# Kernel tuning notes

Hardware: AMD Instinct MI355X
Metric: run time of the kernel (lower is better)

Reference implementation:

```python
import jax, jax.numpy as jnp
import numpy as np

B, N, D, H = 1, 4096, 1024, 16
E = D // H  # head_dim = 64


def setup_inputs() -> dict:
    key = jax.random.key(0)
    ks = jax.random.split(key, 5)
    s = 0.02
    return {
        "query": jax.random.normal(ks[0], (B, N, D), dtype=jnp.float32),
        "Wq": jax.random.normal(ks[1], (D, D), dtype=jnp.float32) * s,
        "Wk": jax.random.normal(ks[2], (D, D), dtype=jnp.float32) * s,
        "Wv": jax.random.normal(ks[3], (D, D), dtype=jnp.float32) * s,
        "Wo": jax.random.normal(ks[4], (D, D), dtype=jnp.float32) * s,
        "bo": jnp.zeros((D,), dtype=jnp.float32),
    }


def reference(query, Wq, Wk, Wv, Wo, bo):
    # self-attention: key = value = query
    # nn.Linear: y = x @ W.T  (weights stored as [out, in])
    q = query @ Wq.T  # [b, n, d]
    k = query @ Wk.T
    v = query @ Wv.T
    # 'b n (h e) -> b h n e'
    q = q.reshape(B, N, H, E).transpose(0, 2, 1, 3)
    k = k.reshape(B, N, H, E).transpose(0, 2, 1, 3)
    v = v.reshape(B, N, H, E).transpose(0, 2, 1, 3)
    scale = 1.0 / jnp.sqrt(jnp.asarray(E, dtype=q.dtype))
    attn = jnp.einsum('bhne,bhme->bhnm', q, k) * scale  # [b, h, n, n]
    attn = jax.nn.softmax(attn, axis=-1)
    out = jnp.einsum('bhnm,bhme->bhne', attn, v)  # [b, h, n, e]
    # 'b h n e -> b n (h e)'
    out = out.transpose(0, 2, 1, 3).reshape(B, N, D)
    out = out @ Wo.T + bo
    return out
```

## Files before the change

### kernel.cpp

```cpp
#include <hip/hip_runtime.h>


typedef __attribute__((ext_vector_type(8))) __bf16 bf16x8;
typedef __attribute__((ext_vector_type(4))) float f32x4;
typedef __attribute__((ext_vector_type(16))) float f32x16;
typedef __attribute__((ext_vector_type(4))) unsigned short us4;
typedef __attribute__((ext_vector_type(4))) unsigned int u32x4;
typedef __attribute__((ext_vector_type(2))) unsigned int u32x2;

#define DEV __device__ __forceinline__

#define QSCALE 0.1803368801111204f

DEV unsigned short f2bf(float x) {
  union { float f; unsigned u; } c; c.f = x;
  unsigned u = c.u;
  u += 0x7FFFu + ((u >> 16) & 1u);
  return (unsigned short)(u >> 16);
}

DEV float expq(float x) {
#if __has_builtin(__builtin_amdgcn_exp2f)
  return __builtin_amdgcn_exp2f(x);
#else
  float r;
  asm("v_exp_f32 %0, %1" : "=v"(r) : "v"(x));
  return r;
#endif
}

DEV unsigned cvtpk_bf16(float lo, float hi) {
  unsigned r;
  asm("v_cvt_pk_bf16_f32 %0, %1, %2" : "=v"(r) : "v"(lo), "v"(hi));
  return r;
}

DEV void plswap_u(unsigned& a, unsigned& b) {
#if __has_builtin(__builtin_amdgcn_permlane32_swap)
  u32x2 r = __builtin_amdgcn_permlane32_swap(a, b, false, false);
  a = r.x; b = r.y;
#else
  asm("v_permlane32_swap_b32 %0, %1" : "+v"(a), "+v"(b));
#endif
}

DEV void gload16(const void* g, void* lds) {
  __builtin_amdgcn_global_load_lds(
      (const __attribute__((address_space(1))) unsigned int*)g,
      (__attribute__((address_space(3))) unsigned int*)lds, 16, 0, 0);
}

__global__ void cast_all(const float* __restrict__ q,
                         const float* __restrict__ wa,
                         const float* __restrict__ wb,
                         const float* __restrict__ wc,
                         const float* __restrict__ wd,
                         unsigned short* __restrict__ qo,
                         unsigned short* __restrict__ wout) {
  const int y = blockIdx.y;
  const int i = blockIdx.x * 256 + threadIdx.x;
  const float* src;
  unsigned short* dst;
  if (y < 4) {
    src = q + (size_t)y * 1048576;
    dst = qo + (size_t)y * 1048576;
  } else {
    src = (y == 4) ? wa : (y == 5) ? wb : (y == 6) ? wc : wd;
    dst = wout + (size_t)(y - 4) * 1048576;
  }
  float4 v = reinterpret_cast<const float4*>(src)[i];
  us4 o;
  o.x = f2bf(v.x); o.y = f2bf(v.y); o.z = f2bf(v.z); o.w = f2bf(v.w);
  reinterpret_cast<us4*>(dst)[i] = o;
}

__global__ __launch_bounds__(256)
void gemm_qkv(const unsigned short* __restrict__ A,
              const unsigned short* __restrict__ B,
              unsigned short* __restrict__ Qo,
              unsigned short* __restrict__ Ko,
              unsigned short* __restrict__ Vo) {
  constexpr int K = 1024, BK = 64;
  __shared__ unsigned short As[128 * BK];
  __shared__ unsigned short Bs[128 * BK];
  const int t = threadIdx.x;
  const int w = t >> 6, l = t & 63;
  const int brow = blockIdx.x * 128;
  const int bcol = blockIdx.y * 128;
  const int wr = w >> 1, wc = w & 1;
  const int lr = l >> 3;
  const int lc = ((l & 7) ^ lr) * 8;
  const int fr = l & 15;
  const int fcb = (l >> 4) * 16;
  const int swz = (l & 7) << 4;

  f32x4 acc[4][4] = {};
  const char* Asb = (const char*)As;
  const char* Bsb = (const char*)Bs;

  for (int k0 = 0; k0 < K; k0 += BK) {
#pragma unroll
    for (int i = 0; i < 4; ++i) {
      const int r = w * 32 + i * 8;
      gload16(A + (size_t)(brow + r + lr) * K + k0 + lc, (void*)(As + r * BK));
      gload16(B + (size_t)(bcol + r + lr) * K + k0 + lc, (void*)(Bs + r * BK));
    }
    __syncthreads();
#pragma unroll
    for (int kk = 0; kk < 2; ++kk) {
      bf16x8 af[4], bfr[4];
#pragma unroll
      for (int m = 0; m < 4; ++m)
        af[m] = *(const bf16x8*)(Asb + (wr * 64 + m * 16 + fr) * 128 +
                                 ((kk * 64 + fcb) ^ swz));
#pragma unroll
      for (int n = 0; n < 4; ++n)
        bfr[n] = *(const bf16x8*)(Bsb + (wc * 64 + n * 16 + fr) * 128 +
                                  ((kk * 64 + fcb) ^ swz));
#pragma unroll
      for (int m = 0; m < 4; ++m)
#pragma unroll
        for (int n = 0; n < 4; ++n)
          acc[m][n] = __builtin_amdgcn_mfma_f32_16x16x32_bf16(
              af[m], bfr[n], acc[m][n], 0, 0, 0);
    }
    __syncthreads();
  }

  const int seg = blockIdx.y >> 3;
  const int orow = brow + wr * 64 + (l >> 4) * 4;
  const int ocol = (blockIdx.y & 7) * 128 + wc * 64 + fr;
  if (seg == 1) {
#pragma unroll
    for (int n = 0; n < 4; ++n) {
      const int C = ocol + n * 16;
      const int bn = (C >> 6) * 262144 + ((C & 63) >> 3) * 512 + (C & 7);
#pragma unroll
      for (int m = 0; m < 4; ++m)
#pragma unroll
        for (int j = 0; j < 4; ++j) {
          const int R = orow + m * 16 + j;
          Ko[bn + (R >> 6) * 4096 + (R & 63) * 8] = f2bf(acc[m][n][j]);
        }
    }
  } else if (seg == 2) {
#pragma unroll
    for (int n = 0; n < 4; ++n) {
      const int C = ocol + n * 16;
      const int bn = (C >> 6) * 262144 + (C & 63) * 8;
#pragma unroll
      for (int m = 0; m < 4; ++m)
#pragma unroll
        for (int j = 0; j < 4; ++j) {
          const int R = orow + m * 16 + j;
          Vo[bn + (R >> 6) * 4096 + ((R & 63) >> 3) * 512 + (R & 7)] =
              f2bf(acc[m][n][j]);
        }
    }
  } else {
#pragma unroll
    for (int m = 0; m < 4; ++m)
#pragma unroll
      for (int n = 0; n < 4; ++n)
#pragma unroll
        for (int j = 0; j < 4; ++j)
          Qo[(size_t)(orow + m * 16 + j) * 1024 + (ocol + n * 16)] =
              f2bf(acc[m][n][j] * QSCALE);
  }
}

__global__ __launch_bounds__(256)
void gemm_out64(const unsigned short* __restrict__ A,
                const unsigned short* __restrict__ B,
                float* __restrict__ C, const float* __restrict__ bias) {
  constexpr int N = 1024, K = 1024, BK = 64;
  __shared__ unsigned short As[64 * BK];
  __shared__ unsigned short Bs[128 * BK];
  const int t = threadIdx.x;
  const int w = t >> 6, l = t & 63;
  const int brow = blockIdx.x * 64;
  const int bcol = blockIdx.y * 128;
  const int wr = w >> 1, wc = w & 1;
  const int lr = l >> 3;
  const int lc = ((l & 7) ^ lr) * 8;
  const int fr = l & 15;
  const int fcb = (l >> 4) * 16;
  const int swz = (l & 7) << 4;

  f32x4 acc[2][4] = {};
  const char* Asb = (const char*)As;
  const char* Bsb = (const char*)Bs;

  for (int k0 = 0; k0 < K; k0 += BK) {
#pragma unroll
    for (int i = 0; i < 2; ++i) {
      const int r = w * 16 + i * 8;
      gload16(A + (size_t)(brow + r + lr) * K + k0 + lc, (void*)(As + r * BK));
    }
#pragma unroll
    for (int i = 0; i < 4; ++i) {
      const int r = w * 32 + i * 8;
      gload16(B + (size_t)(bcol + r + lr) * K + k0 + lc, (void*)(Bs + r * BK));
    }
    __syncthreads();
#pragma unroll
    for (int kk = 0; kk < 2; ++kk) {
      bf16x8 af[2], bfr[4];
#pragma unroll
      for (int m = 0; m < 2; ++m)
        af[m] = *(const bf16x8*)(Asb + (wr * 32 + m * 16 + fr) * 128 +
                                 ((kk * 64 + fcb) ^ swz));
#pragma unroll
      for (int n = 0; n < 4; ++n)
        bfr[n] = *(const bf16x8*)(Bsb + (wc * 64 + n * 16 + fr) * 128 +
                                  ((kk * 64 + fcb) ^ swz));
#pragma unroll
      for (int m = 0; m < 2; ++m)
#pragma unroll
        for (int n = 0; n < 4; ++n)
          acc[m][n] = __builtin_amdgcn_mfma_f32_16x16x32_bf16(
              af[m], bfr[n], acc[m][n], 0, 0, 0);
    }
    __syncthreads();
  }

  const int orow = brow + wr * 32 + (l >> 4) * 4;
  const int ocol = bcol + wc * 64 + fr;
#pragma unroll
  for (int m = 0; m < 2; ++m)
#pragma unroll
    for (int n = 0; n < 4; ++n)
#pragma unroll
      for (int j = 0; j < 4; ++j)
        C[(size_t)(orow + m * 16 + j) * N + (ocol + n * 16)] =
            acc[m][n][j] + bias[ocol + n * 16];
}

__global__ __launch_bounds__(512, 4)
void attn_v9(const unsigned short* __restrict__ Q,
             const unsigned short* __restrict__ Kp,
             const unsigned short* __restrict__ Vp,
             unsigned short* __restrict__ AO) {
  constexpr int N = 4096, D = 1024, NT = N / 64;
  __shared__ unsigned long long LDSA[65536 / 8];
  char* LDS = (char*)LDSA;
  const int t = threadIdx.x, w = t >> 6, l = t & 63;
  const int g = w >> 2, wg = w & 3;
  const int flat = blockIdx.x;
  const int c = flat & 7, ii = flat >> 3;
  const int h = c * 2 + (ii >> 5);
  const int qt = ii & 31;
  const int q0 = qt * 128 + wg * 32;
  const int ln = l & 31, hi = l >> 5;
  const int lr = l >> 3;
  const int ko = hi * 1024 + ln * 16;

  char* kb0 = LDS + (g * 2 + 0) * 8192;
  char* kb1 = LDS + (g * 2 + 1) * 8192;
  char* vb0 = LDS + 32768 + (g * 2 + 0) * 8192;
  char* vb1 = LDS + 32768 + (g * 2 + 1) * 8192;

  bf16x8 qf[4];
  {
    const unsigned short* qp = Q + (size_t)(q0 + ln) * D + h * 64 + hi * 8;
#pragma unroll
    for (int ks = 0; ks < 4; ++ks) qf[ks] = *(const bf16x8*)(qp + ks * 16);
  }
  bf16x8 onesf;
  {
    u32x4 ov = {0x3F803F80u, 0x3F803F80u, 0x3F803F80u, 0x3F803F80u};
    onesf = __builtin_bit_cast(bf16x8, ov);
  }

  f32x16 oacc0 = {}, oacc1 = {}, dsum = {};

  const int stoff = wg * 2048;
  const char* Kg = (const char*)Kp + ((size_t)(h * 64 + g)) * 8192 + stoff + l * 16;
  const char* Vg = (const char*)Vp + ((size_t)(h * 64 + g)) * 8192 + stoff + l * 16;

  auto stage = [&](char* kd, char* vd, int it) {
    const size_t o = (size_t)it * 16384;
    gload16(Kg + o, kd + stoff);
    gload16(Kg + o + 1024, kd + stoff + 1024);
    gload16(Vg + o, vd + stoff);
    gload16(Vg + o + 1024, vd + stoff + 1024);
  };

  stage(kb0, vb0, 0);
  __syncthreads();

  for (int i = 0; i < NT / 2; ++i) {
    const char* ksb = (i & 1) ? kb1 : kb0;
    const char* vsb = (i & 1) ? vb1 : vb0;
    if (i + 1 < NT / 2)
      stage((i & 1) ? kb0 : kb1, (i & 1) ? vb0 : vb1, i + 1);

    f32x16 sa = {}, sb = {};
    __builtin_amdgcn_s_setprio(1);
#pragma unroll
    for (int ks = 0; ks < 4; ++ks) {
      bf16x8 kf0 = *(const bf16x8*)(ksb + ks * 2048 + ko);
      bf16x8 kf1 = *(const bf16x8*)(ksb + ks * 2048 + 512 + ko);
      sa = __builtin_amdgcn_mfma_f32_32x32x16_bf16(kf0, qf[ks], sa, 0, 0, 0);
      sb = __builtin_amdgcn_mfma_f32_32x32x16_bf16(kf1, qf[ks], sb, 0, 0, 0);
    }
    __builtin_amdgcn_s_setprio(0);

#pragma unroll
    for (int r = 0; r < 16; ++r) { sa[r] = expq(sa[r]); sb[r] = expq(sb[r]); }

    unsigned pw[4][4];
#pragma unroll
    for (int kvs = 0; kvs < 4; ++kvs) {
      const f32x16& S = (kvs < 2) ? sa : sb;
      const int rb = (kvs & 1) * 8;
      unsigned A0 = cvtpk_bf16(S[rb + 0], S[rb + 1]);
      unsigned B0 = cvtpk_bf16(S[rb + 4], S[rb + 5]);
      unsigned A1 = cvtpk_bf16(S[rb + 2], S[rb + 3]);
      unsigned B1 = cvtpk_bf16(S[rb + 6], S[rb + 7]);
      plswap_u(A0, B0);
      plswap_u(A1, B1);
      pw[kvs][0] = A0; pw[kvs][1] = A1; pw[kvs][2] = B0; pw[kvs][3] = B1;
    }

    __builtin_amdgcn_s_setprio(1);
#pragma unroll
    for (int kvs = 0; kvs < 4; ++kvs) {
      u32x4 pv = {pw[kvs][0], pw[kvs][1], pw[kvs][2], pw[kvs][3]};
      bf16x8 pf = __builtin_bit_cast(bf16x8, pv);
      bf16x8 vf0 = *(const bf16x8*)(vsb + kvs * 2048 + ko);
      bf16x8 vf1 = *(const bf16x8*)(vsb + kvs * 2048 + 512 + ko);
      dsum = __builtin_amdgcn_mfma_f32_32x32x16_bf16(onesf, pf, dsum, 0, 0, 0);
      oacc0 = __builtin_amdgcn_mfma_f32_32x32x16_bf16(vf0, pf, oacc0, 0, 0, 0);
      oacc1 = __builtin_amdgcn_mfma_f32_32x32x16_bf16(vf1, pf, oacc1, 0, 0, 0);
    }
    __builtin_amdgcn_s_setprio(0);

    __syncthreads();
  }

  float* cb = (float*)LDS;
  float* cl = (float*)(LDS + 32768);
  if (g == 1) {
    float* p = cb + (wg * 64 + l) * 32;
#pragma unroll
    for (int r = 0; r < 16; ++r) { p[r] = oacc0[r]; p[16 + r] = oacc1[r]; }
    cl[wg * 64 + l] = dsum[0];
  }
  __syncthreads();
  if (g == 0) {
    float* p = cb + (wg * 64 + l) * 32;
#pragma unroll
    for (int r = 0; r < 16; ++r) { oacc0[r] += p[r]; oacc1[r] += p[16 + r]; }
    const float inv = 1.0f / (dsum[0] + cl[wg * 64 + l]);

    char* Osc = LDS + 34816 + wg * 4096;
#pragma unroll
    for (int es = 0; es < 2; ++es)
#pragma unroll
      for (int gg = 0; gg < 4; ++gg)
#pragma unroll
        for (int c2 = 0; c2 < 2; ++c2) {
          const f32x16& oa = es == 0 ? oacc0 : oacc1;
          unsigned pk = cvtpk_bf16(oa[gg * 4 + c2 * 2] * inv,
                                   oa[gg * 4 + c2 * 2 + 1] * inv);
          const int col = es * 64 + gg * 16 + hi * 8 + c2 * 4;
          *(unsigned*)(Osc + ln * 128 + (col ^ ((ln & 7) << 4))) = pk;
        }
#pragma unroll
    for (int p2 = 0; p2 < 4; ++p2) {
      const int q = p2 * 8 + lr;
      bf16x8 ov = *(const bf16x8*)(Osc + q * 128 + (((l & 7) ^ lr) << 4));
      *(bf16x8*)(AO + (size_t)(q0 + q) * D + h * 64 + (l & 7) * 8) = ov;
    }
  }
}

extern "C" void kernel_launch(void* const* d_in, const int* in_sizes, int n_in,
                              void* d_out, int out_size, void* d_ws, size_t ws_size,
                              hipStream_t stream) {
  const float* query = (const float*)d_in[0];
  const float* Wq    = (const float*)d_in[1];
  const float* Wk    = (const float*)d_in[2];
  const float* Wv    = (const float*)d_in[3];
  const float* Wo    = (const float*)d_in[4];
  const float* bo    = (const float*)d_in[5];
  float* out = (float*)d_out;

  char* ws = (char*)d_ws;
  const size_t MB = 1024 * 1024;
  unsigned short* Wqkv_b = (unsigned short*)(ws + 0 * MB);
  unsigned short* Wo_b   = (unsigned short*)(ws + 6 * MB);
  unsigned short* Xb     = (unsigned short*)(ws + 8 * MB);
  unsigned short* Qb     = (unsigned short*)(ws + 16 * MB);
  unsigned short* Kb     = (unsigned short*)(ws + 24 * MB);
  unsigned short* Vtb    = (unsigned short*)(ws + 40 * MB);
  unsigned short* AOb    = (unsigned short*)(ws + 32 * MB);

  cast_all<<<dim3(1024, 8), dim3(256), 0, stream>>>(query, Wq, Wk, Wv, Wo,
                                                    Xb, Wqkv_b);

  gemm_qkv<<<dim3(32, 24), dim3(256), 0, stream>>>(Xb, Wqkv_b, Qb, Kb, Vtb);

  attn_v9<<<dim3(512), dim3(512), 0, stream>>>(Qb, Kb, Vtb, AOb);

  gemm_out64<<<dim3(64, 8), dim3(256), 0, stream>>>(AOb, Wo_b, out, bo);
}
```

Before: 148.1 us.

## Split attention KV loop four ways with smaller query tiles and retiled K/V layout

The attention kernel now gives each block a 64-row query tile, split as two waves of 32 rows, instead of 128 rows. The eight waves form four KV-split groups of two, each processing 32-key chunks, and the grid grows to 1024 blocks. The QKV GEMM epilogue writes K and V in a 32-row-chunk packed layout to match. The aim is more parallelism and less per-iteration register pressure. The cost is more redundant K/V loads across blocks and a three-way partial-sum reduction through LDS at the end.

```diff
diff --git a/kernel.cpp b/kernel.cpp
--- a/kernel.cpp
+++ b/kernel.cpp
@@ -134,13 +134,13 @@
 #pragma unroll
     for (int n = 0; n < 4; ++n) {
       const int C = ocol + n * 16;
-      const int bn = (C >> 6) * 262144 + ((C & 63) >> 3) * 512 + (C & 7);
+      const int bn = (C >> 6) * 262144 + ((C & 63) >> 3) * 256 + (C & 7);
 #pragma unroll
       for (int m = 0; m < 4; ++m)
 #pragma unroll
         for (int j = 0; j < 4; ++j) {
           const int R = orow + m * 16 + j;
-          Ko[bn + (R >> 6) * 4096 + (R & 63) * 8] = f2bf(acc[m][n][j]);
+          Ko[bn + (R >> 5) * 2048 + (R & 31) * 8] = f2bf(acc[m][n][j]);
         }
     }
   } else if (seg == 2) {
@@ -153,7 +153,7 @@
 #pragma unroll
         for (int j = 0; j < 4; ++j) {
           const int R = orow + m * 16 + j;
-          Vo[bn + (R >> 6) * 4096 + ((R & 63) >> 3) * 512 + (R & 7)] =
+          Vo[bn + (R >> 5) * 2048 + ((R & 31) >> 3) * 512 + (R & 7)] =
               f2bf(acc[m][n][j]);
         }
     }
@@ -237,28 +237,25 @@
 }
 
 __global__ __launch_bounds__(512, 4)
-void attn_v9(const unsigned short* __restrict__ Q,
-             const unsigned short* __restrict__ Kp,
-             const unsigned short* __restrict__ Vp,
-             unsigned short* __restrict__ AO) {
-  constexpr int N = 4096, D = 1024, NT = N / 64;
+void attn_v10(const unsigned short* __restrict__ Q,
+              const unsigned short* __restrict__ Kp,
+              const unsigned short* __restrict__ Vp,
+              unsigned short* __restrict__ AO) {
+  constexpr int D = 1024, NIT = 32;
   __shared__ unsigned long long LDSA[65536 / 8];
   char* LDS = (char*)LDSA;
   const int t = threadIdx.x, w = t >> 6, l = t & 63;
-  const int g = w >> 2, wg = w & 3;
+  const int g = w >> 1, wq = w & 1;
   const int flat = blockIdx.x;
   const int c = flat & 7, ii = flat >> 3;
-  const int h = c * 2 + (ii >> 5);
-  const int qt = ii & 31;
-  const int q0 = qt * 128 + wg * 32;
+  const int h = c * 2 + (ii >> 6);
+  const int qt = ii & 63;
+  const int q0 = qt * 64 + wq * 32;
   const int ln = l & 31, hi = l >> 5;
   const int lr = l >> 3;
-  const int ko = hi * 1024 + ln * 16;
-
-  char* kb0 = LDS + (g * 2 + 0) * 8192;
-  char* kb1 = LDS + (g * 2 + 1) * 8192;
-  char* vb0 = LDS + 32768 + (g * 2 + 0) * 8192;
-  char* vb1 = LDS + 32768 + (g * 2 + 1) * 8192;
+
+  char* kbuf = LDS + g * 8192;
+  char* vbuf = LDS + 32768 + g * 8192;
 
   bf16x8 qf[4];
   {
@@ -274,50 +271,47 @@
 
   f32x16 oacc0 = {}, oacc1 = {}, dsum = {};
 
-  const int stoff = wg * 2048;
-  const char* Kg = (const char*)Kp + ((size_t)(h * 64 + g)) * 8192 + stoff + l * 16;
-  const char* Vg = (const char*)Vp + ((size_t)(h * 64 + g)) * 8192 + stoff + l * 16;
-
-  auto stage = [&](char* kd, char* vd, int it) {
+  const char* Kg = (const char*)Kp + ((size_t)(h * 128 + g)) * 4096 + wq * 2048 + l * 16;
+  const char* Vg = (const char*)Vp + ((size_t)(h * 128 + g)) * 4096 + wq * 2048 + l * 16;
+
+  auto stage = [&](int buf, int it) {
     const size_t o = (size_t)it * 16384;
-    gload16(Kg + o, kd + stoff);
-    gload16(Kg + o + 1024, kd + stoff + 1024);
-    gload16(Vg + o, vd + stoff);
-    gload16(Vg + o + 1024, vd + stoff + 1024);
+    char* kd = kbuf + buf * 4096 + wq * 2048;
+    char* vd = vbuf + buf * 4096 + wq * 2048;
+    gload16(Kg + o, kd);
+    gload16(Kg + o + 1024, kd + 1024);
+    gload16(Vg + o, vd);
+    gload16(Vg + o + 1024, vd + 1024);
   };
 
-  stage(kb0, vb0, 0);
+  stage(0, 0);
   __syncthreads();
 
-  for (int i = 0; i < NT / 2; ++i) {
-    const char* ksb = (i & 1) ? kb1 : kb0;
-    const char* vsb = (i & 1) ? vb1 : vb0;
-    if (i + 1 < NT / 2)
-      stage((i & 1) ? kb0 : kb1, (i & 1) ? vb0 : vb1, i + 1);
-
-    f32x16 sa = {}, sb = {};
+  for (int i = 0; i < NIT; ++i) {
+    const char* ksb = kbuf + (i & 1) * 4096;
+    const char* vsb = vbuf + (i & 1) * 4096;
+    if (i + 1 < NIT) stage((i & 1) ^ 1, i + 1);
+
+    f32x16 sa = {};
     __builtin_amdgcn_s_setprio(1);
 #pragma unroll
     for (int ks = 0; ks < 4; ++ks) {
-      bf16x8 kf0 = *(const bf16x8*)(ksb + ks * 2048 + ko);
-      bf16x8 kf1 = *(const bf16x8*)(ksb + ks * 2048 + 512 + ko);
-      sa = __builtin_amdgcn_mfma_f32_32x32x16_bf16(kf0, qf[ks], sa, 0, 0, 0);
-      sb = __builtin_amdgcn_mfma_f32_32x32x16_bf16(kf1, qf[ks], sb, 0, 0, 0);
+      bf16x8 kf = *(const bf16x8*)(ksb + (ks * 2 + hi) * 512 + ln * 16);
+      sa = __builtin_amdgcn_mfma_f32_32x32x16_bf16(kf, qf[ks], sa, 0, 0, 0);
     }
     __builtin_amdgcn_s_setprio(0);
 
 #pragma unroll
-    for (int r = 0; r < 16; ++r) { sa[r] = expq(sa[r]); sb[r] = expq(sb[r]); }
-
-    unsigned pw[4][4];
-#pragma unroll
-    for (int kvs = 0; kvs < 4; ++kvs) {
-      const f32x16& S = (kvs < 2) ? sa : sb;
-      const int rb = (kvs & 1) * 8;
-      unsigned A0 = cvtpk_bf16(S[rb + 0], S[rb + 1]);
-      unsigned B0 = cvtpk_bf16(S[rb + 4], S[rb + 5]);
-      unsigned A1 = cvtpk_bf16(S[rb + 2], S[rb + 3]);
-      unsigned B1 = cvtpk_bf16(S[rb + 6], S[rb + 7]);
+    for (int r = 0; r < 16; ++r) sa[r] = expq(sa[r]);
+
+    unsigned pw[2][4];
+#pragma unroll
+    for (int kvs = 0; kvs < 2; ++kvs) {
+      const int rb = kvs * 8;
+      unsigned A0 = cvtpk_bf16(sa[rb + 0], sa[rb + 1]);
+      unsigned B0 = cvtpk_bf16(sa[rb + 4], sa[rb + 5]);
+      unsigned A1 = cvtpk_bf16(sa[rb + 2], sa[rb + 3]);
+      unsigned B1 = cvtpk_bf16(sa[rb + 6], sa[rb + 7]);
       plswap_u(A0, B0);
       plswap_u(A1, B1);
       pw[kvs][0] = A0; pw[kvs][1] = A1; pw[kvs][2] = B0; pw[kvs][3] = B1;
@@ -325,11 +319,11 @@
 
     __builtin_amdgcn_s_setprio(1);
 #pragma unroll
-    for (int kvs = 0; kvs < 4; ++kvs) {
+    for (int kvs = 0; kvs < 2; ++kvs) {
       u32x4 pv = {pw[kvs][0], pw[kvs][1], pw[kvs][2], pw[kvs][3]};
       bf16x8 pf = __builtin_bit_cast(bf16x8, pv);
-      bf16x8 vf0 = *(const bf16x8*)(vsb + kvs * 2048 + ko);
-      bf16x8 vf1 = *(const bf16x8*)(vsb + kvs * 2048 + 512 + ko);
+      bf16x8 vf0 = *(const bf16x8*)(vsb + (kvs * 2 + hi) * 1024 + ln * 16);
+      bf16x8 vf1 = *(const bf16x8*)(vsb + (kvs * 2 + hi) * 1024 + 512 + ln * 16);
       dsum = __builtin_amdgcn_mfma_f32_32x32x16_bf16(onesf, pf, dsum, 0, 0, 0);
       oacc0 = __builtin_amdgcn_mfma_f32_32x32x16_bf16(vf0, pf, oacc0, 0, 0, 0);
       oacc1 = __builtin_amdgcn_mfma_f32_32x32x16_bf16(vf1, pf, oacc1, 0, 0, 0);
@@ -340,21 +334,26 @@
   }
 
   float* cb = (float*)LDS;
-  float* cl = (float*)(LDS + 32768);
-  if (g == 1) {
-    float* p = cb + (wg * 64 + l) * 32;
+  float* cl = (float*)(LDS + 49152);
+  if (g != 0) {
+    float* p = cb + (((g - 1) * 128) + wq * 64 + l) * 32;
 #pragma unroll
     for (int r = 0; r < 16; ++r) { p[r] = oacc0[r]; p[16 + r] = oacc1[r]; }
-    cl[wg * 64 + l] = dsum[0];
+    cl[(g - 1) * 128 + wq * 64 + l] = dsum[0];
   }
   __syncthreads();
   if (g == 0) {
-    float* p = cb + (wg * 64 + l) * 32;
-#pragma unroll
-    for (int r = 0; r < 16; ++r) { oacc0[r] += p[r]; oacc1[r] += p[16 + r]; }
-    const float inv = 1.0f / (dsum[0] + cl[wg * 64 + l]);
-
-    char* Osc = LDS + 34816 + wg * 4096;
+    float tot = dsum[0];
+#pragma unroll
+    for (int gg = 0; gg < 3; ++gg) {
+      float* p = cb + ((gg * 128) + wq * 64 + l) * 32;
+#pragma unroll
+      for (int r = 0; r < 16; ++r) { oacc0[r] += p[r]; oacc1[r] += p[16 + r]; }
+      tot += cl[gg * 128 + wq * 64 + l];
+    }
+    const float inv = 1.0f / tot;
+
+    char* Osc = LDS + 51200 + wq * 4096;
 #pragma unroll
     for (int es = 0; es < 2; ++es)
 #pragma unroll
@@ -402,7 +401,7 @@
 
   gemm_qkv<<<dim3(32, 24), dim3(256), 0, stream>>>(Xb, Wqkv_b, Qb, Kb, Vtb);
 
-  attn_v9<<<dim3(512), dim3(512), 0, stream>>>(Qb, Kb, Vtb, AOb);
+  attn_v10<<<dim3(1024), dim3(512), 0, stream>>>(Qb, Kb, Vtb, AOb);
 
   gemm_out64<<<dim3(64, 8), dim3(256), 0, stream>>>(AOb, Wo_b, out, bo);
 }
```

Result: slower. 160.0 us (+8.1%).

## Load K/V fragments directly from global into registers, drop LDS staging and split-KV

Applied to the files above, without the earlier changes.

The attention kernel no longer stages K and V tiles through LDS with block-wide barriers. Each wave reads its MFMA operand fragments straight from global memory (assumed pre-swizzled), prefetching the next K tile into a ping-pong register set while computing the current one. The two-group KV split and its LDS reduction are removed, so blocks shrink to 4 waves and each wave walks the whole KV range. This removes __syncthreads and LDS traffic but puts more pressure on registers and L2, since each wave fetches K/V itself instead of sharing through LDS, and halves the parallelism per query tile.

```diff
diff --git a/kernel.cpp b/kernel.cpp
--- a/kernel.cpp
+++ b/kernel.cpp
@@ -236,29 +236,71 @@
             acc[m][n][j] + bias[ocol + n * 16];
 }
 
-__global__ __launch_bounds__(512, 4)
-void attn_v9(const unsigned short* __restrict__ Q,
-             const unsigned short* __restrict__ Kp,
-             const unsigned short* __restrict__ Vp,
-             unsigned short* __restrict__ AO) {
-  constexpr int N = 4096, D = 1024, NT = N / 64;
-  __shared__ unsigned long long LDSA[65536 / 8];
-  char* LDS = (char*)LDSA;
+
+#define LOADK(dst, tt) do { \
+    const char* kp_ = Kg + (size_t)(tt) * 8192; \
+    _Pragma("unroll") for (int ks = 0; ks < 4; ++ks) { \
+      dst##0[ks] = *(const bf16x8*)(kp_ + ks * 2048); \
+      dst##1[ks] = *(const bf16x8*)(kp_ + ks * 2048 + 512); \
+    } \
+  } while (0)
+
+#define BODYV11(TT, KCUR, KNXT) do { \
+    const char* vp_ = Vg + (size_t)(TT) * 8192; \
+    bf16x8 vf_[4][2]; \
+    _Pragma("unroll") for (int kvs = 0; kvs < 4; ++kvs) { \
+      vf_[kvs][0] = *(const bf16x8*)(vp_ + kvs * 2048); \
+      vf_[kvs][1] = *(const bf16x8*)(vp_ + kvs * 2048 + 512); \
+    } \
+    if ((TT) + 1 < NT) LOADK(KNXT, (TT) + 1); \
+    f32x16 sa = {}, sb = {}; \
+    __builtin_amdgcn_s_setprio(1); \
+    _Pragma("unroll") for (int ks = 0; ks < 4; ++ks) { \
+      sa = __builtin_amdgcn_mfma_f32_32x32x16_bf16(KCUR##0[ks], qf[ks], sa, 0, 0, 0); \
+      sb = __builtin_amdgcn_mfma_f32_32x32x16_bf16(KCUR##1[ks], qf[ks], sb, 0, 0, 0); \
+    } \
+    __builtin_amdgcn_s_setprio(0); \
+    _Pragma("unroll") for (int r = 0; r < 16; ++r) { \
+      sa[r] = expq(sa[r]); sb[r] = expq(sb[r]); } \
+    unsigned pw[4][4]; \
+    _Pragma("unroll") for (int kvs = 0; kvs < 4; ++kvs) { \
+      const f32x16& S = (kvs < 2) ? sa : sb; \
+      const int rb = (kvs & 1) * 8; \
+      unsigned A0 = cvtpk_bf16(S[rb + 0], S[rb + 1]); \
+      unsigned B0 = cvtpk_bf16(S[rb + 4], S[rb + 5]); \
+      unsigned A1 = cvtpk_bf16(S[rb + 2], S[rb + 3]); \
+      unsigned B1 = cvtpk_bf16(S[rb + 6], S[rb + 7]); \
+      plswap_u(A0, B0); \
+      plswap_u(A1, B1); \
+      pw[kvs][0] = A0; pw[kvs][1] = A1; pw[kvs][2] = B0; pw[kvs][3] = B1; \
+    } \
+    __builtin_amdgcn_s_setprio(1); \
+    _Pragma("unroll") for (int kvs = 0; kvs < 4; ++kvs) { \
+      u32x4 pv = {pw[kvs][0], pw[kvs][1], pw[kvs][2], pw[kvs][3]}; \
+      bf16x8 pf = __builtin_bit_cast(bf16x8, pv); \
+      dsum = __builtin_amdgcn_mfma_f32_32x32x16_bf16(onesf, pf, dsum, 0, 0, 0); \
+      oacc0 = __builtin_amdgcn_mfma_f32_32x32x16_bf16(vf_[kvs][0], pf, oacc0, 0, 0, 0); \
+      oacc1 = __builtin_amdgcn_mfma_f32_32x32x16_bf16(vf_[kvs][1], pf, oacc1, 0, 0, 0); \
+    } \
+    __builtin_amdgcn_s_setprio(0); \
+  } while (0)
+
+__global__ __launch_bounds__(256, 2)
+void attn_v11(const unsigned short* __restrict__ Q,
+              const unsigned short* __restrict__ Kp,
+              const unsigned short* __restrict__ Vp,
+              unsigned short* __restrict__ AO) {
+  constexpr int D = 1024, NT = 64;
+  __shared__ char LDS[16384];
   const int t = threadIdx.x, w = t >> 6, l = t & 63;
-  const int g = w >> 2, wg = w & 3;
   const int flat = blockIdx.x;
   const int c = flat & 7, ii = flat >> 3;
   const int h = c * 2 + (ii >> 5);
   const int qt = ii & 31;
-  const int q0 = qt * 128 + wg * 32;
+  const int q0 = qt * 128 + w * 32;
   const int ln = l & 31, hi = l >> 5;
   const int lr = l >> 3;
   const int ko = hi * 1024 + ln * 16;
-
-  char* kb0 = LDS + (g * 2 + 0) * 8192;
-  char* kb1 = LDS + (g * 2 + 1) * 8192;
-  char* vb0 = LDS + 32768 + (g * 2 + 0) * 8192;
-  char* vb1 = LDS + 32768 + (g * 2 + 1) * 8192;
 
   bf16x8 qf[4];
   {
@@ -274,105 +316,36 @@
 
   f32x16 oacc0 = {}, oacc1 = {}, dsum = {};
 
-  const int stoff = wg * 2048;
-  const char* Kg = (const char*)Kp + ((size_t)(h * 64 + g)) * 8192 + stoff + l * 16;
-  const char* Vg = (const char*)Vp + ((size_t)(h * 64 + g)) * 8192 + stoff + l * 16;
-
-  auto stage = [&](char* kd, char* vd, int it) {
-    const size_t o = (size_t)it * 16384;
-    gload16(Kg + o, kd + stoff);
-    gload16(Kg + o + 1024, kd + stoff + 1024);
-    gload16(Vg + o, vd + stoff);
-    gload16(Vg + o + 1024, vd + stoff + 1024);
-  };
-
-  stage(kb0, vb0, 0);
-  __syncthreads();
-
-  for (int i = 0; i < NT / 2; ++i) {
-    const char* ksb = (i & 1) ? kb1 : kb0;
-    const char* vsb = (i & 1) ? vb1 : vb0;
-    if (i + 1 < NT / 2)
-      stage((i & 1) ? kb0 : kb1, (i & 1) ? vb0 : vb1, i + 1);
-
-    f32x16 sa = {}, sb = {};
-    __builtin_amdgcn_s_setprio(1);
-#pragma unroll
-    for (int ks = 0; ks < 4; ++ks) {
-      bf16x8 kf0 = *(const bf16x8*)(ksb + ks * 2048 + ko);
-      bf16x8 kf1 = *(const bf16x8*)(ksb + ks * 2048 + 512 + ko);
-      sa = __builtin_amdgcn_mfma_f32_32x32x16_bf16(kf0, qf[ks], sa, 0, 0, 0);
-      sb = __builtin_amdgcn_mfma_f32_32x32x16_bf16(kf1, qf[ks], sb, 0, 0, 0);
-    }
-    __builtin_amdgcn_s_setprio(0);
-
-#pragma unroll
-    for (int r = 0; r < 16; ++r) { sa[r] = expq(sa[r]); sb[r] = expq(sb[r]); }
-
-    unsigned pw[4][4];
-#pragma unroll
-    for (int kvs = 0; kvs < 4; ++kvs) {
-      const f32x16& S = (kvs < 2) ? sa : sb;
-      const int rb = (kvs & 1) * 8;
-      unsigned A0 = cvtpk_bf16(S[rb + 0], S[rb + 1]);
-      unsigned B0 = cvtpk_bf16(S[rb + 4], S[rb + 5]);
-      unsigned A1 = cvtpk_bf16(S[rb + 2], S[rb + 3]);
-      unsigned B1 = cvtpk_bf16(S[rb + 6], S[rb + 7]);
-      plswap_u(A0, B0);
-      plswap_u(A1, B1);
-      pw[kvs][0] = A0; pw[kvs][1] = A1; pw[kvs][2] = B0; pw[kvs][3] = B1;
-    }
-
-    __builtin_amdgcn_s_setprio(1);
-#pragma unroll
-    for (int kvs = 0; kvs < 4; ++kvs) {
-      u32x4 pv = {pw[kvs][0], pw[kvs][1], pw[kvs][2], pw[kvs][3]};
-      bf16x8 pf = __builtin_bit_cast(bf16x8, pv);
-      bf16x8 vf0 = *(const bf16x8*)(vsb + kvs * 2048 + ko);
-      bf16x8 vf1 = *(const bf16x8*)(vsb + kvs * 2048 + 512 + ko);
-      dsum = __builtin_amdgcn_mfma_f32_32x32x16_bf16(onesf, pf, dsum, 0, 0, 0);
-      oacc0 = __builtin_amdgcn_mfma_f32_32x32x16_bf16(vf0, pf, oacc0, 0, 0, 0);
-      oacc1 = __builtin_amdgcn_mfma_f32_32x32x16_bf16(vf1, pf, oacc1, 0, 0, 0);
-    }
-    __builtin_amdgcn_s_setprio(0);
-
-    __syncthreads();
-  }
-
-  float* cb = (float*)LDS;
-  float* cl = (float*)(LDS + 32768);
-  if (g == 1) {
-    float* p = cb + (wg * 64 + l) * 32;
-#pragma unroll
-    for (int r = 0; r < 16; ++r) { p[r] = oacc0[r]; p[16 + r] = oacc1[r]; }
-    cl[wg * 64 + l] = dsum[0];
-  }
-  __syncthreads();
-  if (g == 0) {
-    float* p = cb + (wg * 64 + l) * 32;
-#pragma unroll
-    for (int r = 0; r < 16; ++r) { oacc0[r] += p[r]; oacc1[r] += p[16 + r]; }
-    const float inv = 1.0f / (dsum[0] + cl[wg * 64 + l]);
-
-    char* Osc = LDS + 34816 + wg * 4096;
-#pragma unroll
-    for (int es = 0; es < 2; ++es)
-#pragma unroll
-      for (int gg = 0; gg < 4; ++gg)
-#pragma unroll
-        for (int c2 = 0; c2 < 2; ++c2) {
-          const f32x16& oa = es == 0 ? oacc0 : oacc1;
-          unsigned pk = cvtpk_bf16(oa[gg * 4 + c2 * 2] * inv,
-                                   oa[gg * 4 + c2 * 2 + 1] * inv);
-          const int col = es * 64 + gg * 16 + hi * 8 + c2 * 4;
-          *(unsigned*)(Osc + ln * 128 + (col ^ ((ln & 7) << 4))) = pk;
-        }
-#pragma unroll
-    for (int p2 = 0; p2 < 4; ++p2) {
-      const int q = p2 * 8 + lr;
-      bf16x8 ov = *(const bf16x8*)(Osc + q * 128 + (((l & 7) ^ lr) << 4));
-      *(bf16x8*)(AO + (size_t)(q0 + q) * D + h * 64 + (l & 7) * 8) = ov;
-    }
+  const char* Kg = (const char*)Kp + (size_t)(h * 64) * 8192 + ko;
+  const char* Vg = (const char*)Vp + (size_t)(h * 64) * 8192 + ko;
+
+  bf16x8 kA0[4], kA1[4], kB0[4], kB1[4];
+  LOADK(kA, 0);
+
+  for (int tt = 0; tt < NT; tt += 2) {
+    BODYV11(tt, kA, kB);
+    BODYV11(tt + 1, kB, kA);
+  }
+
+  const float inv = 1.0f / dsum[0];
+  char* Osc = LDS + w * 4096;
+#pragma unroll
+  for (int es = 0; es < 2; ++es)
+#pragma unroll
+    for (int gg = 0; gg < 4; ++gg)
+#pragma unroll
+      for (int c2 = 0; c2 < 2; ++c2) {
+        const f32x16& oa = es == 0 ? oacc0 : oacc1;
+        unsigned pk = cvtpk_bf16(oa[gg * 4 + c2 * 2] * inv,
+                                 oa[gg * 4 + c2 * 2 + 1] * inv);
+        const int col = es * 64 + gg * 16 + hi * 8 + c2 * 4;
+        *(unsigned*)(Osc + ln * 128 + (col ^ ((ln & 7) << 4))) = pk;
+      }
+#pragma unroll
+  for (int p2 = 0; p2 < 4; ++p2) {
+    const int q = p2 * 8 + lr;
+    bf16x8 ov = *(const bf16x8*)(Osc + q * 128 + (((l & 7) ^ lr) << 4));
+    *(bf16x8*)(AO + (size_t)(q0 + q) * D + h * 64 + (l & 7) * 8) = ov;
   }
 }
 
@@ -402,7 +375,7 @@
 
   gemm_qkv<<<dim3(32, 24), dim3(256), 0, stream>>>(Xb, Wqkv_b, Qb, Kb, Vtb);
 
-  attn_v9<<<dim3(512), dim3(512), 0, stream>>>(Qb, Kb, Vtb, AOb);
+  attn_v11<<<dim3(512), dim3(256), 0, stream>>>(Qb, Kb, Vtb, AOb);
 
   gemm_out64<<<dim3(64, 8), dim3(256), 0, stream>>>(AOb, Wo_b, out, bo);
 }
```

After: 160.5 us. 8.4% more time.

## Load V straight to registers and compute row sums with VALU instead of MFMA

Applied to the files above, without the earlier changes.

The attention kernel stops staging V tiles through LDS and loads each wave's V fragments directly from global memory into registers at the top of every iteration. LDS then holds only the double-buffered K tiles. The softmax denominator is now accumulated with a per-lane VALU add tree over the exponentiated scores, and a permlane32 swap at the end combines the two half-waves, replacing the extra ones-vector MFMA per key slice. This removes one third of the PV-stage MFMAs and the V LDS traffic, but exposes global-load latency for V inside the loop and adds register pressure.

```diff
diff --git a/kernel.cpp b/kernel.cpp
--- a/kernel.cpp
+++ b/kernel.cpp
@@ -42,6 +42,12 @@
 #else
   asm("v_permlane32_swap_b32 %0, %1" : "+v"(a), "+v"(b));
 #endif
+}
+
+DEV void plswap_f(float& a, float& b) {
+  unsigned ua = __float_as_uint(a), ub = __float_as_uint(b);
+  plswap_u(ua, ub);
+  a = __uint_as_float(ua); b = __uint_as_float(ub);
 }
 
 DEV void gload16(const void* g, void* lds) {
@@ -237,12 +243,12 @@
 }
 
 __global__ __launch_bounds__(512, 4)
-void attn_v9(const unsigned short* __restrict__ Q,
-             const unsigned short* __restrict__ Kp,
-             const unsigned short* __restrict__ Vp,
-             unsigned short* __restrict__ AO) {
-  constexpr int N = 4096, D = 1024, NT = N / 64;
-  __shared__ unsigned long long LDSA[65536 / 8];
+void attn_v13(const unsigned short* __restrict__ Q,
+              const unsigned short* __restrict__ Kp,
+              const unsigned short* __restrict__ Vp,
+              unsigned short* __restrict__ AO) {
+  constexpr int D = 1024, NIT = 32;
+  __shared__ unsigned long long LDSA[51200 / 8];
   char* LDS = (char*)LDSA;
   const int t = threadIdx.x, w = t >> 6, l = t & 63;
   const int g = w >> 2, wg = w & 3;
@@ -257,8 +263,6 @@
 
   char* kb0 = LDS + (g * 2 + 0) * 8192;
   char* kb1 = LDS + (g * 2 + 1) * 8192;
-  char* vb0 = LDS + 32768 + (g * 2 + 0) * 8192;
-  char* vb1 = LDS + 32768 + (g * 2 + 1) * 8192;
 
   bf16x8 qf[4];
   {
@@ -266,34 +270,34 @@
 #pragma unroll
     for (int ks = 0; ks < 4; ++ks) qf[ks] = *(const bf16x8*)(qp + ks * 16);
   }
-  bf16x8 onesf;
-  {
-    u32x4 ov = {0x3F803F80u, 0x3F803F80u, 0x3F803F80u, 0x3F803F80u};
-    onesf = __builtin_bit_cast(bf16x8, ov);
-  }
-
-  f32x16 oacc0 = {}, oacc1 = {}, dsum = {};
+
+  f32x16 oacc0 = {}, oacc1 = {};
+  float lsum = 0.f;
 
   const int stoff = wg * 2048;
-  const char* Kg = (const char*)Kp + ((size_t)(h * 64 + g)) * 8192 + stoff + l * 16;
-  const char* Vg = (const char*)Vp + ((size_t)(h * 64 + g)) * 8192 + stoff + l * 16;
-
-  auto stage = [&](char* kd, char* vd, int it) {
+  const char* Kg = (const char*)Kp + (size_t)(h * 64 + g) * 8192 + stoff + l * 16;
+  const char* Vg = (const char*)Vp + (size_t)(h * 64 + g) * 8192 + ko;
+
+  auto stageK = [&](char* kd, int it) {
     const size_t o = (size_t)it * 16384;
     gload16(Kg + o, kd + stoff);
     gload16(Kg + o + 1024, kd + stoff + 1024);
-    gload16(Vg + o, vd + stoff);
-    gload16(Vg + o + 1024, vd + stoff + 1024);
   };
 
-  stage(kb0, vb0, 0);
+  stageK(kb0, 0);
   __syncthreads();
 
-  for (int i = 0; i < NT / 2; ++i) {
+  for (int i = 0; i < NIT; ++i) {
     const char* ksb = (i & 1) ? kb1 : kb0;
-    const char* vsb = (i & 1) ? vb1 : vb0;
-    if (i + 1 < NT / 2)
-      stage((i & 1) ? kb0 : kb1, (i & 1) ? vb0 : vb1, i + 1);
+
+    const char* vp = Vg + (size_t)i * 16384;
+    bf16x8 vf[4][2];
+#pragma unroll
+    for (int kvs = 0; kvs < 4; ++kvs) {
+      vf[kvs][0] = *(const bf16x8*)(vp + kvs * 2048);
+      vf[kvs][1] = *(const bf16x8*)(vp + kvs * 2048 + 512);
+    }
+    if (i + 1 < NIT) stageK((i & 1) ? kb0 : kb1, i + 1);
 
     f32x16 sa = {}, sb = {};
     __builtin_amdgcn_s_setprio(1);
@@ -308,6 +312,16 @@
 
 #pragma unroll
     for (int r = 0; r < 16; ++r) { sa[r] = expq(sa[r]); sb[r] = expq(sb[r]); }
+    {
+      float red[16];
+#pragma unroll
+      for (int r = 0; r < 16; ++r) red[r] = sa[r] + sb[r];
+#pragma unroll
+      for (int s = 8; s >= 1; s >>= 1)
+#pragma unroll
+        for (int r = 0; r < s; ++r) red[r] += red[r + s];
+      lsum += red[0];
+    }
 
     unsigned pw[4][4];
 #pragma unroll
@@ -328,11 +342,8 @@
     for (int kvs = 0; kvs < 4; ++kvs) {
       u32x4 pv = {pw[kvs][0], pw[kvs][1], pw[kvs][2], pw[kvs][3]};
       bf16x8 pf = __builtin_bit_cast(bf16x8, pv);
-      bf16x8 vf0 = *(const bf16x8*)(vsb + kvs * 2048 + ko);
-      bf16x8 vf1 = *(const bf16x8*)(vsb + kvs * 2048 + 512 + ko);
-      dsum = __builtin_amdgcn_mfma_f32_32x32x16_bf16(onesf, pf, dsum, 0, 0, 0);
-      oacc0 = __builtin_amdgcn_mfma_f32_32x32x16_bf16(vf0, pf, oacc0, 0, 0, 0);
-      oacc1 = __builtin_amdgcn_mfma_f32_32x32x16_bf16(vf1, pf, oacc1, 0, 0, 0);
+      oacc0 = __builtin_amdgcn_mfma_f32_32x32x16_bf16(vf[kvs][0], pf, oacc0, 0, 0, 0);
+      oacc1 = __builtin_amdgcn_mfma_f32_32x32x16_bf16(vf[kvs][1], pf, oacc1, 0, 0, 0);
     }
     __builtin_amdgcn_s_setprio(0);
 
@@ -345,14 +356,17 @@
     float* p = cb + (wg * 64 + l) * 32;
 #pragma unroll
     for (int r = 0; r < 16; ++r) { p[r] = oacc0[r]; p[16 + r] = oacc1[r]; }
-    cl[wg * 64 + l] = dsum[0];
+    cl[wg * 64 + l] = lsum;
   }
   __syncthreads();
   if (g == 0) {
     float* p = cb + (wg * 64 + l) * 32;
 #pragma unroll
     for (int r = 0; r < 16; ++r) { oacc0[r] += p[r]; oacc1[r] += p[16 + r]; }
-    const float inv = 1.0f / (dsum[0] + cl[wg * 64 + l]);
+    lsum += cl[wg * 64 + l];
+    float sa2 = lsum, sb2 = lsum;
+    plswap_f(sa2, sb2);
+    const float inv = 1.0f / (sa2 + sb2);
 
     char* Osc = LDS + 34816 + wg * 4096;
 #pragma unroll
@@ -402,7 +416,7 @@
 
   gemm_qkv<<<dim3(32, 24), dim3(256), 0, stream>>>(Xb, Wqkv_b, Qb, Kb, Vtb);
 
-  attn_v9<<<dim3(512), dim3(512), 0, stream>>>(Qb, Kb, Vtb, AOb);
+  attn_v13<<<dim3(512), dim3(512), 0, stream>>>(Qb, Kb, Vtb, AOb);
 
   gemm_out64<<<dim3(64, 8), dim3(256), 0, stream>>>(AOb, Wo_b, out, bo);
 }
```

Measured after the change: 178.1 us. 1.2x slower.
